# Kernel optimization log

Measured on AMD Instinct MI355X. Metric: run time of the kernel, lower is better.

The kernel has to match this reference:

```python
import jax, jax.numpy as jnp
import numpy as np

B = 4096          # batch of samples
M = 128           # n_orbitals
F = 32            # n_fermions
H = 512           # hidden_units


def setup_inputs() -> dict:
    key = jax.random.key(0)
    kn, kphi, kw1, kb1, kw2, kb2 = jax.random.split(key, 6)
    # occupancy strings: exactly F ones among M orbitals per sample
    keys = jax.random.split(kn, B)
    occ_idx = jax.vmap(lambda k: jax.random.permutation(k, M)[:F])(keys)  # [B,F]
    n = jnp.zeros((B, M), jnp.float32).at[jnp.arange(B)[:, None], occ_idx].set(1.0)
    # parameters
    Phi = jax.random.normal(kphi, (F, M), jnp.float32) * 0.1
    W1 = jax.random.normal(kw1, (M, H), jnp.float32) / np.sqrt(M)
    b1 = jnp.zeros((H,), jnp.float32)
    W2 = jax.random.normal(kw2, (H, F * M), jnp.float32) / np.sqrt(H)
    b2 = jnp.zeros((F * M,), jnp.float32)
    return {"n": n, "Phi": Phi, "W1": W1, "b1": b1, "W2": W2, "b2": b2}


def reference(n, Phi, W1, b1, W2, b2):
    # backflow MLP: Dense -> tanh -> Dense, reshaped to (F, M) per sample
    h = jnp.tanh(n @ W1 + b1)                       # [B,H]
    bf = (h @ W2 + b2).reshape(-1, F, M)            # [B,F,M]
    kernel = Phi[None] + bf                         # [B,F,M]
    # occupied orbital columns; exactly F ones per row, top_k is stable so
    # indices come out in ascending order (same as jnp.where(n, size=F))
    idx = jax.lax.top_k(n, F)[1]                    # [B,F] int32
    phi = jnp.take_along_axis(kernel, idx[:, None, :], axis=2)  # [B,F,F]
    sign, logabs = jnp.linalg.slogdet(phi)
    return jnp.log(sign.astype(jnp.complex64)) + logabs.astype(jnp.complex64)  # [B] complex
```

## Files before the change

kernel.cpp:

```cpp
#include <hip/hip_runtime.h>
#include <hip/hip_bf16.h>
#include <math.h>

#define B_N 4096
#define M_N 128
#define F_N 32
#define H_N 512
#define NFM 4096

#define WAVE_SYNC() do { \
  asm volatile("s_waitcnt lgkmcnt(0)" ::: "memory"); \
  __builtin_amdgcn_sched_barrier(0); \
} while (0)

__global__ __launch_bounds__(256) void k_pre(
    const float* __restrict__ n, const float* __restrict__ W1,
    const float* __restrict__ b1, const float* __restrict__ W2,
    float* __restrict__ W2t, float* __restrict__ h_ws,
    unsigned int* __restrict__ mask)
{
  __shared__ float s_buf[32 * 132];
  __shared__ int s_idx[2][F_N];
  __shared__ int s_cnt0[2];

  const int t = threadIdx.x;

  if (blockIdx.x < 512) {
    const int k = blockIdx.x;
    #pragma unroll
    for (int i = 0; i < 4; ++i) {
      int m0 = i * 1024 + t * 4;
      float4 v = *(const float4*)&W2[(size_t)k * NFM + m0];
      int ig = m0 >> 7, c = m0 & 127;
      s_buf[ig * 132 + c + 0] = v.x;
      s_buf[ig * 132 + c + 1] = v.y;
      s_buf[ig * 132 + c + 2] = v.z;
      s_buf[ig * 132 + c + 3] = v.w;
    }
    __syncthreads();
    const int c  = t >> 1;
    const int ih = (t & 1) * 16;
    float* outp = W2t + (size_t)c * (H_N * F_N) + k * F_N + ih;
    #pragma unroll
    for (int i = 0; i < 4; ++i) {
      int ig = ih + i * 4;
      float4 v = make_float4(s_buf[(ig+0)*132 + c], s_buf[(ig+1)*132 + c],
                             s_buf[(ig+2)*132 + c], s_buf[(ig+3)*132 + c]);
      *(float4*)(outp + i * 4) = v;
    }
    return;
  }

  const int half = t >> 7;
  const int tl   = t & 127;
  const int b    = (blockIdx.x - 512) * 2 + half;
  const int lane = t & 63;

  {
    float v = n[(size_t)b * M_N + tl];
    bool p = v > 0.5f;
    unsigned long long m = __ballot(p);
    int before = __popcll(m & ((1ull << lane) - 1ull));
    if (lane == 0) {
      int w2 = (tl < 64) ? 0 : 2;
      mask[b*4 + w2 + 0] = (unsigned)m;
      mask[b*4 + w2 + 1] = (unsigned)(m >> 32);
    }
    if (tl < 64) {
      if (lane == 0) s_cnt0[half] = __popcll(m);
      if (p) s_idx[half][before] = tl;
    }
    __syncthreads();
    if (tl >= 64 && p) s_idx[half][s_cnt0[half] + before] = tl;
    __syncthreads();
  }

  const int c0 = tl * 4;
  float4 acc = make_float4(0.f, 0.f, 0.f, 0.f);
  #pragma unroll
  for (int j = 0; j < F_N; ++j) {
    float4 wv = *(const float4*)&W1[(size_t)s_idx[half][j] * H_N + c0];
    acc.x += wv.x; acc.y += wv.y; acc.z += wv.z; acc.w += wv.w;
  }
  float4 bv = *(const float4*)&b1[c0];
  acc.x = tanhf(acc.x + bv.x);
  acc.y = tanhf(acc.y + bv.y);
  acc.z = tanhf(acc.z + bv.z);
  acc.w = tanhf(acc.w + bv.w);
  *(float4*)&h_ws[(size_t)b * H_N + c0] = acc;
}

__global__ __launch_bounds__(512) void k_fill(
    const unsigned int* __restrict__ mask,
    int* __restrict__ bcnt, int* __restrict__ boff,
    int* __restrict__ bent, int* __restrict__ loc)
{
  const int c = blockIdx.x;
  const int t = threadIdx.x;
  const int w = t >> 6, lane = t & 63;
  const int word = c >> 5, bit = c & 31;
  __shared__ int s_wcnt[64];
  __shared__ int s_pre[64];
  __shared__ int s_red[16];

  int cnt_loc = 0, off_loc = 0;
  #pragma unroll 1
  for (int ch = 0; ch < 8; ++ch) {
    const int b = ch * 512 + t;
    unsigned m0 = mask[(size_t)b*4+0], m1 = mask[(size_t)b*4+1];
    unsigned m2 = mask[(size_t)b*4+2], m3 = mask[(size_t)b*4+3];
    unsigned wv = (word == 0) ? m0 : (word == 1) ? m1 : (word == 2) ? m2 : m3;
    bool p = (wv >> bit) & 1u;
    int r = __popc(wv & ((1u << bit) - 1u));
    if (word > 0) r += __popc(m0);
    if (word > 1) r += __popc(m1);
    if (word > 2) r += __popc(m2);
    unsigned long long bal = __ballot(p);
    if (lane == 0) s_wcnt[ch * 8 + w] = __popcll(bal);
    cnt_loc += (int)p;
    off_loc += r;
  }
  #pragma unroll
  for (int off = 32; off > 0; off >>= 1) {
    cnt_loc += __shfl_down(cnt_loc, off);
    off_loc += __shfl_down(off_loc, off);
  }
  if (lane == 0) { s_red[w] = cnt_loc; s_red[8 + w] = off_loc; }
  __syncthreads();
  int cnt_tot = 0, off_tot = 0;
  #pragma unroll
  for (int i = 0; i < 8; ++i) { cnt_tot += s_red[i]; off_tot += s_red[8 + i]; }
  if (t == 0) {
    bcnt[c] = cnt_tot; boff[c] = off_tot;
    int run = 0;
    #pragma unroll
    for (int i = 0; i < 64; ++i) { s_pre[i] = run; run += s_wcnt[i]; }
  }
  __syncthreads();

  #pragma unroll 1
  for (int ch = 0; ch < 8; ++ch) {
    const int b = ch * 512 + t;
    unsigned m0 = mask[(size_t)b*4+0], m1 = mask[(size_t)b*4+1];
    unsigned m2 = mask[(size_t)b*4+2], m3 = mask[(size_t)b*4+3];
    unsigned wv = (word == 0) ? m0 : (word == 1) ? m1 : (word == 2) ? m2 : m3;
    bool p = (wv >> bit) & 1u;
    int j = __popc(wv & ((1u << bit) - 1u));
    if (word > 0) j += __popc(m0);
    if (word > 1) j += __popc(m1);
    if (word > 2) j += __popc(m2);
    unsigned long long bal = __ballot(p);
    int before = __popcll(bal & ((1ull << lane) - 1ull));
    if (p) {
      int pos = s_pre[ch * 8 + w] + before;
      bent[(size_t)c * B_N + pos] = (b << 5) | j;
      loc[b * 32 + j] = off_tot + pos;
    }
  }
}

__global__ __launch_bounds__(256) void k2_gemm_gather(
    const float* __restrict__ h, const float* __restrict__ W2t,
    const float* __restrict__ b2, const float* __restrict__ Phi,
    const int* __restrict__ bcnt, const int* __restrict__ boff,
    const int* __restrict__ bent, float* __restrict__ phi_bucket)
{
  __shared__ __align__(16) float smem[2 * 2624];
  __shared__ int s_b[128];

  const int tid = threadIdx.x;
  const int c   = blockIdx.x;
  const int cnt = bcnt[c];
  const int t0  = blockIdx.y * 128;
  if (t0 >= cnt) return;
  const int base = boff[c];
  const float* w2tc = W2t + (size_t)c * (H_N * F_N);

  if (tid < 128) {
    int ii = t0 + tid;
    int e  = bent[(size_t)c * B_N + (ii < cnt ? ii : cnt - 1)];
    s_b[tid] = e >> 5;
  }
  __syncthreads();

  const int kA  = tid & 15;
  const int rbA = (tid >> 4) * 8;
  const int tx  = tid & 7;
  const int tyr = tid >> 3;

  int rowb[8];
  #pragma unroll
  for (int i = 0; i < 8; ++i) rowb[i] = s_b[rbA + i];

  float acc[4][4];
  #pragma unroll
  for (int i = 0; i < 4; ++i)
    #pragma unroll
    for (int u = 0; u < 4; ++u) acc[i][u] = 0.f;

  float aReg[8], bReg0, bReg1;

  #pragma unroll
  for (int i = 0; i < 8; ++i)
    aReg[i] = h[(size_t)rowb[i] * H_N + kA];
  bReg0 = w2tc[tid];
  bReg1 = w2tc[256 + tid];
  *(float4*)&smem[kA * 132 + rbA] =
      make_float4(aReg[0], aReg[1], aReg[2], aReg[3]);
  *(float4*)&smem[kA * 132 + rbA + 4] =
      make_float4(aReg[4], aReg[5], aReg[6], aReg[7]);
  smem[2112 + tid] = bReg0;
  smem[2112 + 256 + tid] = bReg1;
  __syncthreads();

  #pragma unroll 1
  for (int t = 0; t < 32; ++t) {
    float* Atc = smem + (t & 1) * 2624;
    float* Btc = Atc + 2112;
    float* Atn = smem + ((t + 1) & 1) * 2624;
    float* Btn = Atn + 2112;

    if (t < 31) {
      int k0n = (t + 1) * 16;
      #pragma unroll
      for (int i = 0; i < 8; ++i)
        aReg[i] = h[(size_t)rowb[i] * H_N + k0n + kA];
      bReg0 = w2tc[k0n * 32 + tid];
      bReg1 = w2tc[k0n * 32 + 256 + tid];
    }

    #pragma unroll
    for (int kk = 0; kk < 16; ++kk) {
      float4 av = *(const float4*)&Atc[kk * 132 + tyr * 4];
      float4 bv = *(const float4*)&Btc[kk * 32 + tx * 4];
      float a4[4] = {av.x, av.y, av.z, av.w};
      float b4[4] = {bv.x, bv.y, bv.z, bv.w};
      #pragma unroll
      for (int i = 0; i < 4; ++i)
        #pragma unroll
        for (int u = 0; u < 4; ++u)
          acc[i][u] = fmaf(a4[i], b4[u], acc[i][u]);
    }

    if (t < 31) {
      *(float4*)&Atn[kA * 132 + rbA] =
          make_float4(aReg[0], aReg[1], aReg[2], aReg[3]);
      *(float4*)&Atn[kA * 132 + rbA + 4] =
          make_float4(aReg[4], aReg[5], aReg[6], aReg[7]);
      Btn[tid] = bReg0;
      Btn[256 + tid] = bReg1;
      __syncthreads();
    }
  }

  #pragma unroll
  for (int i = 0; i < 4; ++i) {
    int r = tyr * 4 + i;
    if (t0 + r < cnt) {
      int col = base + t0 + r;
      float v[4];
      #pragma unroll
      for (int u = 0; u < 4; ++u) {
        int ig   = tx * 4 + u;
        int colw = ig * M_N + c;
        v[u] = Phi[colw] + (acc[i][u] + b2[colw]);
      }
      *(float4*)&phi_bucket[(size_t)col * 32 + tx * 4] =
          make_float4(v[0], v[1], v[2], v[3]);
    }
  }
}

__global__ __launch_bounds__(256) void k3_det(
    const float* __restrict__ phi_bucket, const int* __restrict__ loc,
    float* __restrict__ out)
{
  __shared__ float A[4][32 * 33];
  const int w = threadIdx.x >> 6;
  const int lane = threadIdx.x & 63;
  const int b = blockIdx.x * 4 + w;
  float* Aw = A[w];

  {
    const int jj = lane & 31;
    const int hi = lane >> 5;
    int lcol = loc[b * 32 + jj];
    const float* colp = phi_bucket + (size_t)lcol * 32 + hi * 16;
    #pragma unroll
    for (int i = 0; i < 4; ++i) {
      float4 v = *(const float4*)(colp + i * 4);
      int ig = hi * 16 + i * 4;
      Aw[(ig + 0) * 33 + jj] = v.x;
      Aw[(ig + 1) * 33 + jj] = v.y;
      Aw[(ig + 2) * 33 + jj] = v.z;
      Aw[(ig + 3) * 33 + jj] = v.w;
    }
  }
  WAVE_SYNC();

  float logabs = 0.f;
  int negs = 0;
  for (int k = 0; k < 32; ++k) {
    const int row = lane & 31;
    float v = -1.f;
    int vi = row;
    if (row >= k) v = fabsf(Aw[row * 33 + k]);
    #pragma unroll
    for (int off = 16; off > 0; off >>= 1) {
      float ov = __shfl_xor(v, off);
      int oi = __shfl_xor(vi, off);
      if (ov > v || (ov == v && oi < vi)) { v = ov; vi = oi; }
    }
    int p = vi;
    if (p != k) {
      negs ^= 1;
      if (lane < 32) {
        float tmp = Aw[k * 33 + lane];
        Aw[k * 33 + lane] = Aw[p * 33 + lane];
        Aw[p * 33 + lane] = tmp;
      }
      WAVE_SYNC();
    }
    float piv = Aw[k * 33 + k];
    if (piv < 0.f) negs ^= 1;
    logabs += logf(fabsf(piv));
    if (lane > k && lane < 32) {
      float l = Aw[lane * 33 + k];
      if (fabsf(piv) >= 1.17549435e-38f) l = l * (1.0f / piv);
      else                               l = l / piv;
      Aw[lane * 33 + k] = l;
    }
    WAVE_SYNC();
    {
      const int mid = (k + 33) >> 1;
      const int j   = lane & 31;
      const int ilo = (lane < 32) ? (k + 1) : mid;
      const int ihi = (lane < 32) ? mid : 32;
      if (j > k) {
        float nukj = -Aw[k * 33 + j];
        for (int i = ilo; i < ihi; ++i)
          Aw[i * 33 + j] = fmaf(nukj, Aw[i * 33 + k], Aw[i * 33 + j]);
      }
    }
    WAVE_SYNC();
  }

  if (lane == 0) {
    out[b]       = logabs;
    out[B_N + b] = (negs & 1) ? 3.14159265358979f : 0.0f;
  }
}

extern "C" void kernel_launch(void* const* d_in, const int* in_sizes, int n_in,
                              void* d_out, int out_size, void* d_ws, size_t ws_size,
                              hipStream_t stream) {
  const float* n   = (const float*)d_in[0];
  const float* Phi = (const float*)d_in[1];
  const float* W1  = (const float*)d_in[2];
  const float* b1  = (const float*)d_in[3];
  const float* W2  = (const float*)d_in[4];
  const float* b2  = (const float*)d_in[5];
  float* out = (float*)d_out;

  char* ws = (char*)d_ws;
  float*        h_ws       = (float*)ws;
  float*        phi_bucket = (float*)(ws + (size_t)8  * 1024 * 1024);
  float*        W2t        = (float*)(ws + (size_t)24 * 1024 * 1024);
  unsigned int* mask       = (unsigned int*)(ws + (size_t)32 * 1024 * 1024);
  int*          bent       = (int*)(ws + (size_t)32 * 1024 * 1024 + 65536);
  int*          loc        = (int*)(ws + (size_t)34 * 1024 * 1024 + 65536);
  int*          bcnt       = (int*)(ws + (size_t)34 * 1024 * 1024 + 65536 + 524288);
  int*          boff       = (int*)(ws + (size_t)34 * 1024 * 1024 + 65536 + 524288 + 4096);

  hipLaunchKernelGGL(k_pre, dim3(512 + B_N / 2), dim3(256), 0, stream,
                     n, W1, b1, W2, W2t, h_ws, mask);
  hipLaunchKernelGGL(k_fill, dim3(M_N), dim3(512), 0, stream,
                     mask, bcnt, boff, bent, loc);
  hipLaunchKernelGGL(k2_gemm_gather, dim3(M_N, 32), dim3(256), 0, stream,
                     h_ws, W2t, b2, Phi, bcnt, boff, bent, phi_bucket);
  hipLaunchKernelGGL(k3_det, dim3(B_N / 4), dim3(256), 0, stream,
                     phi_bucket, loc, out);
}
```

Baseline: 173.0 us.

## Shrink gather-GEMM blocks to single wave with 64-row tiles and wave-level sync

```diff
diff --git a/kernel.cpp b/kernel.cpp
--- a/kernel.cpp
+++ b/kernel.cpp
@@ -159,114 +159,127 @@
   }
 }
 
-__global__ __launch_bounds__(256) void k2_gemm_gather(
+__global__ __launch_bounds__(64) void k2_gemm_gather(
     const float* __restrict__ h, const float* __restrict__ W2t,
     const float* __restrict__ b2, const float* __restrict__ Phi,
     const int* __restrict__ bcnt, const int* __restrict__ boff,
     const int* __restrict__ bent, float* __restrict__ phi_bucket)
 {
-  __shared__ __align__(16) float smem[2 * 2624];
-  __shared__ int s_b[128];
-
-  const int tid = threadIdx.x;
-  const int c   = blockIdx.x;
-  const int cnt = bcnt[c];
-  const int t0  = blockIdx.y * 128;
+  __shared__ __align__(16) float smem[2 * 800];
+  __shared__ int s_b[64];
+
+  const int lane = threadIdx.x;
+  const int c    = blockIdx.x;
+  const int cnt  = bcnt[c];
+  const int t0   = blockIdx.y * 64;
   if (t0 >= cnt) return;
   const int base = boff[c];
   const float* w2tc = W2t + (size_t)c * (H_N * F_N);
 
-  if (tid < 128) {
-    int ii = t0 + tid;
+  {
+    int ii = t0 + lane;
     int e  = bent[(size_t)c * B_N + (ii < cnt ? ii : cnt - 1)];
-    s_b[tid] = e >> 5;
-  }
-  __syncthreads();
-
-  const int kA  = tid & 15;
-  const int rbA = (tid >> 4) * 8;
-  const int tx  = tid & 7;
-  const int tyr = tid >> 3;
+    s_b[lane] = e >> 5;
+  }
+  WAVE_SYNC();
+
+  const int kA  = lane & 7;
+  const int tyr = lane >> 3;
+  const int tx  = lane & 7;
+  const int r8  = tyr * 8;
 
   int rowb[8];
   #pragma unroll
-  for (int i = 0; i < 8; ++i) rowb[i] = s_b[rbA + i];
-
-  float acc[4][4];
-  #pragma unroll
-  for (int i = 0; i < 4; ++i)
+  for (int i = 0; i < 8; ++i) rowb[i] = s_b[r8 + i];
+
+  float acc[8][4];
+  #pragma unroll
+  for (int i = 0; i < 8; ++i)
     #pragma unroll
     for (int u = 0; u < 4; ++u) acc[i][u] = 0.f;
 
-  float aReg[8], bReg0, bReg1;
+  float aReg[8], bReg0, bReg1, bReg2, bReg3;
 
   #pragma unroll
   for (int i = 0; i < 8; ++i)
     aReg[i] = h[(size_t)rowb[i] * H_N + kA];
-  bReg0 = w2tc[tid];
-  bReg1 = w2tc[256 + tid];
-  *(float4*)&smem[kA * 132 + rbA] =
+  bReg0 = w2tc[lane];
+  bReg1 = w2tc[64 + lane];
+  bReg2 = w2tc[128 + lane];
+  bReg3 = w2tc[192 + lane];
+  *(float4*)&smem[kA * 68 + r8] =
       make_float4(aReg[0], aReg[1], aReg[2], aReg[3]);
-  *(float4*)&smem[kA * 132 + rbA + 4] =
+  *(float4*)&smem[kA * 68 + r8 + 4] =
       make_float4(aReg[4], aReg[5], aReg[6], aReg[7]);
-  smem[2112 + tid] = bReg0;
-  smem[2112 + 256 + tid] = bReg1;
-  __syncthreads();
+  smem[544 + lane]       = bReg0;
+  smem[544 + 64 + lane]  = bReg1;
+  smem[544 + 128 + lane] = bReg2;
+  smem[544 + 192 + lane] = bReg3;
+  WAVE_SYNC();
 
   #pragma unroll 1
-  for (int t = 0; t < 32; ++t) {
-    float* Atc = smem + (t & 1) * 2624;
-    float* Btc = Atc + 2112;
-    float* Atn = smem + ((t + 1) & 1) * 2624;
-    float* Btn = Atn + 2112;
-
-    if (t < 31) {
-      int k0n = (t + 1) * 16;
+  for (int t = 0; t < 64; ++t) {
+    float* Atc = smem + (t & 1) * 800;
+    float* Btc = Atc + 544;
+    float* Atn = smem + ((t + 1) & 1) * 800;
+    float* Btn = Atn + 544;
+
+    if (t < 63) {
+      int k0n = (t + 1) * 8;
       #pragma unroll
       for (int i = 0; i < 8; ++i)
         aReg[i] = h[(size_t)rowb[i] * H_N + k0n + kA];
-      bReg0 = w2tc[k0n * 32 + tid];
-      bReg1 = w2tc[k0n * 32 + 256 + tid];
-    }
-
-    #pragma unroll
-    for (int kk = 0; kk < 16; ++kk) {
-      float4 av = *(const float4*)&Atc[kk * 132 + tyr * 4];
+      bReg0 = w2tc[k0n * 32 + lane];
+      bReg1 = w2tc[k0n * 32 + 64 + lane];
+      bReg2 = w2tc[k0n * 32 + 128 + lane];
+      bReg3 = w2tc[k0n * 32 + 192 + lane];
+    }
+
+    #pragma unroll
+    for (int kk = 0; kk < 8; ++kk) {
+      float4 a0 = *(const float4*)&Atc[kk * 68 + r8];
+      float4 a1 = *(const float4*)&Atc[kk * 68 + r8 + 4];
       float4 bv = *(const float4*)&Btc[kk * 32 + tx * 4];
-      float a4[4] = {av.x, av.y, av.z, av.w};
+      float a8[8] = {a0.x, a0.y, a0.z, a0.w, a1.x, a1.y, a1.z, a1.w};
       float b4[4] = {bv.x, bv.y, bv.z, bv.w};
       #pragma unroll
-      for (int i = 0; i < 4; ++i)
+      for (int i = 0; i < 8; ++i)
         #pragma unroll
         for (int u = 0; u < 4; ++u)
-          acc[i][u] = fmaf(a4[i], b4[u], acc[i][u]);
-    }
-
-    if (t < 31) {
-      *(float4*)&Atn[kA * 132 + rbA] =
+          acc[i][u] = fmaf(a8[i], b4[u], acc[i][u]);
+    }
+
+    if (t < 63) {
+      *(float4*)&Atn[kA * 68 + r8] =
           make_float4(aReg[0], aReg[1], aReg[2], aReg[3]);
-      *(float4*)&Atn[kA * 132 + rbA + 4] =
+      *(float4*)&Atn[kA * 68 + r8 + 4] =
           make_float4(aReg[4], aReg[5], aReg[6], aReg[7]);
-      Btn[tid] = bReg0;
-      Btn[256 + tid] = bReg1;
-      __syncthreads();
-    }
-  }
-
-  #pragma unroll
-  for (int i = 0; i < 4; ++i) {
-    int r = tyr * 4 + i;
+      Btn[lane]       = bReg0;
+      Btn[64 + lane]  = bReg1;
+      Btn[128 + lane] = bReg2;
+      Btn[192 + lane] = bReg3;
+      WAVE_SYNC();
+    }
+  }
+
+  float ph[4], bb[4];
+  #pragma unroll
+  for (int u = 0; u < 4; ++u) {
+    int colw = (tx * 4 + u) * M_N + c;
+    ph[u] = Phi[colw];
+    bb[u] = b2[colw];
+  }
+  #pragma unroll
+  for (int i = 0; i < 8; ++i) {
+    int r = r8 + i;
     if (t0 + r < cnt) {
       int col = base + t0 + r;
-      float v[4];
-      #pragma unroll
-      for (int u = 0; u < 4; ++u) {
-        int ig   = tx * 4 + u;
-        int colw = ig * M_N + c;
-        v[u] = Phi[colw] + (acc[i][u] + b2[colw]);
-      }
+      float v0 = ph[0] + (acc[i][0] + bb[0]);
+      float v1 = ph[1] + (acc[i][1] + bb[1]);
+      float v2 = ph[2] + (acc[i][2] + bb[2]);
+      float v3 = ph[3] + (acc[i][3] + bb[3]);
       *(float4*)&phi_bucket[(size_t)col * 32 + tx * 4] =
-          make_float4(v[0], v[1], v[2], v[3]);
+          make_float4(v0, v1, v2, v3);
     }
   }
 }
@@ -376,7 +389,7 @@
                      n, W1, b1, W2, W2t, h_ws, mask);
   hipLaunchKernelGGL(k_fill, dim3(M_N), dim3(512), 0, stream,
                      mask, bcnt, boff, bent, loc);
-  hipLaunchKernelGGL(k2_gemm_gather, dim3(M_N, 32), dim3(256), 0, stream,
+  hipLaunchKernelGGL(k2_gemm_gather, dim3(M_N, 64), dim3(64), 0, stream,
                      h_ws, W2t, b2, Phi, bcnt, boff, bent, phi_bucket);
   hipLaunchKernelGGL(k3_det, dim3(B_N / 4), dim3(256), 0, stream,
                      phi_bucket, loc, out);
```

Result: slower. 183.1 us (+5.8%).
